# Kernel tuning notes

Measured on AMD Instinct MI355X. Metric: run time of the kernel, lower is better.

## Reference

```python
import jax, jax.numpy as jnp
import numpy as np

K0 = 0.7978845608028654  # sqrt(2/pi)
C1 = 0.044715

def _gelu_tanh(x):
    # tanh-approx GELU, matching the Triton kernel's math
    return 0.5 * x * (1.0 + jnp.tanh(K0 * (x + C1 * x * x * x)))

def setup_inputs() -> dict:
    key = jax.random.key(0)
    k1, k2, k3 = jax.random.split(key, 3)
    B, C_in, H, W = 32, 64, 128, 128
    C_out, KH = 128, 3
    x = jax.random.normal(k1, (B, C_in, H, W), dtype=jnp.float32)
    weight = jax.random.normal(k2, (C_out, C_in, KH, KH), dtype=jnp.float32)
    bias = jax.random.normal(k3, (C_out,), dtype=jnp.float32)
    return {"x": x, "weight": weight, "bias": bias}

def reference(x, weight, bias):
    # Valid conv2d, stride 1 (NCHW, OIHW)
    y = jax.lax.conv_general_dilated(
        x, weight,
        window_strides=(1, 1), padding="VALID",
        dimension_numbers=("NCHW", "OIHW", "NCHW"))
    y = y + bias[None, :, None, None]
    y = _gelu_tanh(y)
    # global average pool over spatial dims -> [B, C_out]
    return jnp.mean(y, axis=(2, 3))
```

## Files before the change

kernel.cpp:

```cpp
#include <hip/hip_runtime.h>
#include <cstdint>
#include <cstddef>

#define GK0 0.7978845608028654f
#define GC1 0.044715f

typedef __attribute__((ext_vector_type(8))) short short8;
typedef __attribute__((ext_vector_type(4))) float floatx4;

__device__ __forceinline__ unsigned short f2bf(float f) {
  union { float f; unsigned int u; } v; v.f = f;
  unsigned int r = v.u + 0x7fffu + ((v.u >> 16) & 1u);
  return (unsigned short)(r >> 16);
}

__global__ void k_wt(const float* __restrict__ w, unsigned short* __restrict__ wt) {
  int t = blockIdx.x * 256 + threadIdx.x;
  if (t >= 128 * 64 * 9) return;
  int co = t / 576; int r = t - co * 576; int ci = r / 9; int khw = r - ci * 9;
  wt[(khw * 128 + co) * 64 + ci] = f2bf(w[t]);
}

__global__ __launch_bounds__(256, 4) void k_conv(
    const float* __restrict__ x, const unsigned short* __restrict__ wt,
    const float* __restrict__ bias, float* __restrict__ out) {
  __shared__ unsigned short xs[4 * 66 * 72];
  const int tid = threadIdx.x;
  const int b = blockIdx.z, h0 = blockIdx.y * 2, w0 = blockIdx.x * 64;

  {
    const int ci = tid >> 2, hi = tid & 3;
    const float* src = x + ((size_t)(b * 64 + ci) * 128 + (h0 + hi)) * 128 + w0;
    unsigned short* dst = xs + (hi * 66) * 72 + ci;
#pragma unroll 4
    for (int v = 0; v < 16; v++) {
      float4 f = ((const float4*)src)[v];
      dst[(4 * v + 0) * 72] = f2bf(f.x);
      dst[(4 * v + 1) * 72] = f2bf(f.y);
      dst[(4 * v + 2) * 72] = f2bf(f.z);
      dst[(4 * v + 3) * 72] = f2bf(f.w);
    }
    const bool ok = (w0 == 0);
    dst[64 * 72] = ok ? f2bf(src[64]) : (unsigned short)0;
    dst[65 * 72] = ok ? f2bf(src[65]) : (unsigned short)0;
  }
  __syncthreads();

  const int lane = tid & 63, wave = tid >> 6;
  const int wm = wave & 1, wn = wave >> 1;
  const int m = lane & 15, q = lane >> 4;

  floatx4 acc[4][4];
#pragma unroll
  for (int i = 0; i < 4; i++)
#pragma unroll
    for (int j = 0; j < 4; j++) acc[i][j] = (floatx4){0.f, 0.f, 0.f, 0.f};

  const unsigned short* wbase = wt + ((wm * 64 + m) * 64 + q * 8);
  int bb[4];
#pragma unroll
  for (int nt = 0; nt < 4; nt++) bb[nt] = (wn * 66 + nt * 16 + m) * 72 + q * 8;

  short8 a_cur[4], a_nxt[4];
#pragma unroll
  for (int mt = 0; mt < 4; mt++) a_cur[mt] = *(const short8*)(wbase + mt * 1024);

#pragma unroll
  for (int kk = 0; kk < 18; kk++) {
    const int khw = kk >> 1, cb = (kk & 1) << 5;
    const int kh = khw / 3, kw = khw - kh * 3;
    if (kk < 17) {
      const int khw2 = (kk + 1) >> 1, cb2 = ((kk + 1) & 1) << 5;
      const unsigned short* p = wbase + khw2 * 8192 + cb2;
#pragma unroll
      for (int mt = 0; mt < 4; mt++) a_nxt[mt] = *(const short8*)(p + mt * 1024);
    }
    short8 bf[4];
    const int off = (kh * 66 + kw) * 72 + cb;
#pragma unroll
    for (int nt = 0; nt < 4; nt++) bf[nt] = *(const short8*)(&xs[bb[nt] + off]);
#pragma unroll
    for (int mt = 0; mt < 4; mt++)
#pragma unroll
      for (int nt = 0; nt < 4; nt++)
        acc[mt][nt] = __builtin_amdgcn_mfma_f32_16x16x32_bf16(a_cur[mt], bf[nt], acc[mt][nt], 0, 0, 0);
#pragma unroll
    for (int mt = 0; mt < 4; mt++) a_cur[mt] = a_nxt[mt];
  }

  const float inv_area = 1.0f / (126.0f * 126.0f);
  float* orow = out + b * 128;
#pragma unroll
  for (int mt = 0; mt < 4; mt++) {
#pragma unroll
    for (int r = 0; r < 4; r++) {
      const int co = wm * 64 + mt * 16 + q * 4 + r;
      const float bv = bias[co];
      float s = 0.0f;
#pragma unroll
      for (int nt = 0; nt < 4; nt++) {
        float y = acc[mt][nt][r] + bv;
        float u = GK0 * (y + GC1 * y * y * y);
        float e = __expf(-2.0f * u);
        float g = y * __builtin_amdgcn_rcpf(1.0f + e);
        if (w0 + nt * 16 + m < 126) s += g;
      }
#pragma unroll
      for (int d = 1; d < 16; d <<= 1) s += __shfl_xor(s, d, 64);
      if (m == 0) atomicAdd(&orow[co], s * inv_area);
    }
  }
}

extern "C" void kernel_launch(void* const* d_in, const int* in_sizes, int n_in,
                              void* d_out, int out_size, void* d_ws, size_t ws_size,
                              hipStream_t stream) {
  const float* x    = (const float*)d_in[0];
  const float* w    = (const float*)d_in[1];
  const float* bias = (const float*)d_in[2];
  float* out = (float*)d_out;

  unsigned short* wbuf = (unsigned short*)d_ws;
  if (ws_size < (size_t)9 * 128 * 64 * 2) return;

  hipMemsetAsync(d_out, 0, (size_t)out_size * sizeof(float), stream);
  k_wt<<<288, 256, 0, stream>>>(w, wbuf);
  k_conv<<<dim3(2, 63, 32), 256, 0, stream>>>(x, wbuf, bias, out);
}
```

Before: 397.9 us.

## Restructure input staging to coalesced per-lane loads with vector LDS stores

The input tile loader now has each wave handle one row and each lane one width position, reading 8 channels with strided scalar loads and writing them as one 16-byte vector store to shared memory. This replaces the earlier per-thread float4 reads followed by scattered 2-byte shared stores. The output zeroing moves from a separate memset into the weight-transform kernel, which removes one launch. Launch bounds drop from 4 to 2 blocks per CU, giving the compiler more registers at a possible cost in occupancy. The new global access pattern is coalesced across lanes but issues many more scalar loads per thread.

```diff
diff --git a/kernel.cpp b/kernel.cpp
--- a/kernel.cpp
+++ b/kernel.cpp
@@ -14,39 +14,49 @@
   return (unsigned short)(r >> 16);
 }
 
-__global__ void k_wt(const float* __restrict__ w, unsigned short* __restrict__ wt) {
+__global__ void k_wt(const float* __restrict__ w, unsigned short* __restrict__ wt,
+                     float* __restrict__ out) {
+  if (blockIdx.x == 0) {
+    for (int i = threadIdx.x; i < 32 * 128; i += 256) out[i] = 0.0f;
+  }
   int t = blockIdx.x * 256 + threadIdx.x;
   if (t >= 128 * 64 * 9) return;
   int co = t / 576; int r = t - co * 576; int ci = r / 9; int khw = r - ci * 9;
   wt[(khw * 128 + co) * 64 + ci] = f2bf(w[t]);
 }
 
-__global__ __launch_bounds__(256, 4) void k_conv(
+__global__ __launch_bounds__(256, 2) void k_conv(
     const float* __restrict__ x, const unsigned short* __restrict__ wt,
     const float* __restrict__ bias, float* __restrict__ out) {
   __shared__ unsigned short xs[4 * 66 * 72];
   const int tid = threadIdx.x;
   const int b = blockIdx.z, h0 = blockIdx.y * 2, w0 = blockIdx.x * 64;
+  const int lane = tid & 63, wave = tid >> 6;
 
   {
-    const int ci = tid >> 2, hi = tid & 3;
-    const float* src = x + ((size_t)(b * 64 + ci) * 128 + (h0 + hi)) * 128 + w0;
-    unsigned short* dst = xs + (hi * 66) * 72 + ci;
-#pragma unroll 4
-    for (int v = 0; v < 16; v++) {
-      float4 f = ((const float4*)src)[v];
-      dst[(4 * v + 0) * 72] = f2bf(f.x);
-      dst[(4 * v + 1) * 72] = f2bf(f.y);
-      dst[(4 * v + 2) * 72] = f2bf(f.z);
-      dst[(4 * v + 3) * 72] = f2bf(f.w);
+    const int hi = wave;
+    const float* xrow = x + ((size_t)(b * 64) * 128 + (h0 + hi)) * 128 + w0;
+    unsigned short* dstrow = xs + (hi * 66 + lane) * 72;
+#pragma unroll
+    for (int cc = 0; cc < 8; cc++) {
+      const float* p = xrow + (size_t)cc * 8 * 16384 + lane;
+      short8 v;
+#pragma unroll
+      for (int j = 0; j < 8; j++) v[j] = (short)f2bf(p[(size_t)j * 16384]);
+      *(short8*)(dstrow + cc * 8) = v;
     }
-    const bool ok = (w0 == 0);
-    dst[64 * 72] = ok ? f2bf(src[64]) : (unsigned short)0;
-    dst[65 * 72] = ok ? f2bf(src[65]) : (unsigned short)0;
+    if (lane < 16) {
+      const int e = 64 + (lane & 1), cc = lane >> 1;
+      const bool ok = (w0 + e) < 128;
+      const float* p = x + ((size_t)(b * 64 + cc * 8) * 128 + (h0 + hi)) * 128 + w0 + e;
+      short8 v;
+#pragma unroll
+      for (int j = 0; j < 8; j++) v[j] = ok ? (short)f2bf(p[(size_t)j * 16384]) : (short)0;
+      *(short8*)(xs + (hi * 66 + e) * 72 + cc * 8) = v;
+    }
   }
   __syncthreads();
 
-  const int lane = tid & 63, wave = tid >> 6;
   const int wm = wave & 1, wn = wave >> 1;
   const int m = lane & 15, q = lane >> 4;
 
@@ -123,7 +133,6 @@
   unsigned short* wbuf = (unsigned short*)d_ws;
   if (ws_size < (size_t)9 * 128 * 64 * 2) return;
 
-  hipMemsetAsync(d_out, 0, (size_t)out_size * sizeof(float), stream);
-  k_wt<<<288, 256, 0, stream>>>(w, wbuf);
+  k_wt<<<288, 256, 0, stream>>>(w, wbuf, out);
   k_conv<<<dim3(2, 63, 32), 256, 0, stream>>>(x, wbuf, bias, out);
 }
```

New measurement: 400.2 us. No clear change (+0.6%).
